# Optimization experiments

Hardware: AMD Instinct MI355X
Metric: run time of the kernel (lower is better)

The kernel has to match this reference:

```python
import jax, jax.numpy as jnp
import numpy as np
from jax import lax

B, C_IN, H, W = 32, 2048, 14, 14
C_MID = 1024
EPS = 1e-5


def _bn(x, gamma, beta, mean, var):
    # eval-mode batchnorm over channel axis 1 of NCHW
    inv = gamma / jnp.sqrt(var + EPS)
    return x * inv[None, :, None, None] + (beta - mean * inv)[None, :, None, None]


def setup_inputs() -> dict:
    key = jax.random.key(0)
    ks = jax.random.split(key, 16)
    x = jax.random.normal(ks[0], (B, C_IN, H, W), jnp.float32)
    # conv1: 3x3, 2048 -> 1024, xavier-normal init
    std1 = np.sqrt(2.0 / (C_IN * 9 + C_MID * 9)).astype(np.float32)
    w1 = jax.random.normal(ks[1], (C_MID, C_IN, 3, 3), jnp.float32) * std1
    b1 = jnp.zeros((C_MID,), jnp.float32)
    bn1_gamma = 1.0 + 0.1 * jax.random.normal(ks[2], (C_MID,), jnp.float32)
    bn1_beta = 0.1 * jax.random.normal(ks[3], (C_MID,), jnp.float32)
    bn1_mean = 0.1 * jax.random.normal(ks[4], (C_MID,), jnp.float32)
    bn1_var = jax.random.uniform(ks[5], (C_MID,), jnp.float32, 0.5, 1.5)
    # selectLayer: 1x1, 1024 -> 18 (stored as [out, in])
    std_s = np.sqrt(2.0 / (C_MID + 18)).astype(np.float32)
    w_sel = jax.random.normal(ks[6], (18, C_MID), jnp.float32) * std_s
    b_sel = jnp.zeros((18,), jnp.float32)
    # boxLayer: 1x1, 1024 -> 36, uniform(-5, 5) init
    w_box = jax.random.uniform(ks[7], (36, C_MID), jnp.float32, -5.0, 5.0)
    b_box = jnp.zeros((36,), jnp.float32)
    bnb_gamma = 1.0 + 0.1 * jax.random.normal(ks[8], (36,), jnp.float32)
    bnb_beta = 0.1 * jax.random.normal(ks[9], (36,), jnp.float32)
    bnb_mean = 0.1 * jax.random.normal(ks[10], (36,), jnp.float32)
    bnb_var = jax.random.uniform(ks[11], (36,), jnp.float32, 0.5, 1.5)
    return {
        'x': x, 'w1': w1, 'b1': b1,
        'bn1_gamma': bn1_gamma, 'bn1_beta': bn1_beta, 'bn1_mean': bn1_mean, 'bn1_var': bn1_var,
        'w_sel': w_sel, 'b_sel': b_sel,
        'w_box': w_box, 'b_box': b_box,
        'bnb_gamma': bnb_gamma, 'bnb_beta': bnb_beta, 'bnb_mean': bnb_mean, 'bnb_var': bnb_var,
    }


def reference(x, w1, b1, bn1_gamma, bn1_beta, bn1_mean, bn1_var,
              w_sel, b_sel, w_box, b_box,
              bnb_gamma, bnb_beta, bnb_mean, bnb_var):
    n = x.shape[0]
    # conv1 + BN + ReLU (3x3, padding=1)
    h = lax.conv_general_dilated(x, w1, (1, 1), 'SAME',
                                 dimension_numbers=('NCHW', 'OIHW', 'NCHW'))
    h = h + b1[None, :, None, None]
    h = jax.nn.relu(_bn(h, bn1_gamma, bn1_beta, bn1_mean, bn1_var))
    # selectLayer: 1x1 conv + ReLU -> [n, 18, H, W]
    score = jnp.einsum('nchw,oc->nohw', h, w_sel) + b_sel[None, :, None, None]
    score = jax.nn.relu(score)
    # boxLayer: 1x1 conv + BN + ReLU -> [n, 36, H, W]
    box = jnp.einsum('nchw,oc->nohw', h, w_box) + b_box[None, :, None, None]
    box = jax.nn.relu(_bn(box, bnb_gamma, bnb_beta, bnb_mean, bnb_var))
    # permute NCHW -> NHWC, reshape to anchors
    box = jnp.transpose(box, (0, 2, 3, 1)).reshape(n, -1, 4) * 419.0  # [n, 1764, 4]
    score = jnp.transpose(score, (0, 2, 3, 1)).reshape(n, -1, 2)      # [n, 1764, 2]
    score = jax.nn.softmax(score, axis=-1)
    return score, box
```

## Files before the change

kernel.cpp:

```cpp
#include <hip/hip_runtime.h>
#include <hip/hip_bf16.h>
#include <math.h>

#define CIN   2048
#define CMID  1024
#define NB    32
#define HWSP  196
#define NPOS  6272
#define WELEM 2097152
#define NSTEP 192

typedef __attribute__((ext_vector_type(4))) float f32x4;
typedef __attribute__((ext_vector_type(8))) short short8;
typedef __attribute__((ext_vector_type(4))) float float4v;

typedef const __attribute__((address_space(1))) unsigned int* as1_u32p;
typedef __attribute__((address_space(3))) unsigned int* as3_u32p;

__device__ __forceinline__ void gload_lds16(const void* g, void* l) {
  __builtin_amdgcn_global_load_lds((as1_u32p)g, (as3_u32p)l, 16, 0, 0);
}

__global__ __launch_bounds__(256) void pack_all(
    const float* __restrict__ w1, const float* __restrict__ b1,
    const float* __restrict__ g1, const float* __restrict__ be1,
    const float* __restrict__ mu1, const float* __restrict__ va1,
    const float* __restrict__ wsel, const float* __restrict__ wbox,
    const float* __restrict__ x,
    __hip_bfloat16* __restrict__ Wp, float* __restrict__ inv1,
    float* __restrict__ add1, float* __restrict__ Wh,
    __hip_bfloat16* __restrict__ Xp)
{
  __shared__ char shm[25088];
  if (blockIdx.x < 8192) {
    float* lw = (float*)shm;
    const int gid0 = blockIdx.x * 256;
    const float4v* src4 = (const float4v*)(w1 + (long)gid0 * 9);
    float4v* l4 = (float4v*)lw;
    #pragma unroll
    for (int i = 0; i < 3; ++i) {
      int idx = i * 256 + threadIdx.x;
      if (idx < 576) l4[idx] = src4[idx];
    }
    __syncthreads();
    const int gid = gid0 + threadIdx.x;
    float v[9];
    #pragma unroll
    for (int k = 0; k < 9; ++k) v[k] = lw[threadIdx.x * 9 + k];
    #pragma unroll
    for (int k = 0; k < 9; ++k)
      Wp[(long)k * WELEM + gid] = __float2bfloat16(v[k]);

    if (gid < CMID) {
      float iv = g1[gid] / sqrtf(va1[gid] + 1e-5f);
      inv1[gid] = iv;
      add1[gid] = b1[gid] * iv + be1[gid] - mu1[gid] * iv;
    }
    if (gid < CMID * 54) {
      int co = gid / 54, o = gid % 54;
      Wh[gid] = (o < 18) ? wsel[o * CMID + co] : wbox[(o - 18) * CMID + co];
    }
  } else {
    __hip_bfloat16* lx = (__hip_bfloat16*)shm;
    const int b = blockIdx.x - 8192;
    const int n = b >> 5;
    const int cc = b & 31;
    const int ci0 = cc * 64;
    const float* src = x + ((long)n * CIN + ci0) * HWSP;
    for (int i = threadIdx.x; i < 64 * HWSP; i += 256)
      lx[i] = __float2bfloat16(src[i]);
    __syncthreads();
    const int ci = threadIdx.x & 63;
    const int pq = threadIdx.x >> 6;
    __hip_bfloat16* dst = Xp + (long)n * 256 * CIN + ci0 + ci;
    const __hip_bfloat16 z = __float2bfloat16(0.f);
    #pragma unroll
    for (int k = 0; k < 64; ++k) {
      int pos = k * 4 + pq;
      int y = pos >> 4, xx = pos & 15;
      __hip_bfloat16 v = z;
      if (y >= 1 && y <= 14 && xx >= 1 && xx <= 14)
        v = lx[ci * HWSP + (y - 1) * 14 + (xx - 1)];
      dst[(long)pos * CIN] = v;
    }
  }
}

__global__ __launch_bounds__(256, 2) void conv_mfma(
    const __hip_bfloat16* __restrict__ Wp,
    const __hip_bfloat16* __restrict__ Xp,
    __hip_bfloat16* __restrict__ hout0,
    __hip_bfloat16* __restrict__ hout1,
    __hip_bfloat16* __restrict__ hout2)
{
  __shared__ char smem[2 * 24576];

  const int t = threadIdx.x;
  const int bx = blockIdx.x;
  const int r  = bx & 7;
  const int q  = bx >> 3;
  const int kidx = q >> 2;
  const int mtile = q & 3;
  int ntile;
  if (kidx < 6) {
    ntile = r + 8 * kidx;
  } else {
    if (r != ((q & 3) << 1)) return;
    ntile = 48;
  }
  const int z = blockIdx.y;
  const int lane = t & 63;
  const int wv = t >> 6;
  const int wr2 = wv >> 1;
  const int wc2 = wv & 1;

  const int srow = t >> 2;
  const int swb = ((t & 3) << 4) ^ ((srow & 6) << 3);

  const long arowbase = (long)(mtile * 256 + srow) * CIN + (swb >> 1);

  long bbase[2];
  #pragma unroll
  for (int i = 0; i < 2; ++i) {
    int jj = ntile * 128 + srow + 64 * i;
    int n0 = jj / HWSP, p0 = jj % HWSP;
    int hh = p0 / 14, ww = p0 % 14;
    bbase[i] = (long)(n0 * 256 + hh * 16 + ww) * CIN + (swb >> 1);
  }

  const int fr = lane & 15;
  const int ksl = lane >> 4;
  const int kgsw = ((ksl << 4) ^ ((fr & 6) << 3));

  f32x4 acc[8][4] = {};
  short8 a_[8], b_[4];

  const int tap0 = z * 3;

  #define STAGE(gv, bi) do {                                                    \
    int g_ = (gv);                                                              \
    int kt_ = tap0 + (g_ >> 6);                                                 \
    int ck_ = (g_ & 63) << 5;                                                   \
    int kh_ = (kt_ * 11) >> 5;                                                  \
    int kw_ = kt_ - kh_ * 3;                                                    \
    char* d_ = smem + (bi) * 24576;                                             \
    const __hip_bfloat16* ap_ = Wp + (long)kt_ * WELEM + arowbase + ck_;        \
    _Pragma("unroll")                                                           \
    for (int i_ = 0; i_ < 4; ++i_)                                              \
      gload_lds16(ap_ + (long)i_ * 64 * CIN, d_ + i_ * 4096 + t * 16);          \
    long boff_ = (long)(kh_ * 16 + kw_) * CIN + ck_;                            \
    _Pragma("unroll")                                                           \
    for (int i_ = 0; i_ < 2; ++i_)                                              \
      gload_lds16(Xp + bbase[i_] + boff_, d_ + 16384 + i_ * 4096 + t * 16);     \
  } while (0)

  #define READF(bi) do {                                                        \
    const char* cb_ = smem + (bi) * 24576;                                      \
    _Pragma("unroll")                                                           \
    for (int i = 0; i < 8; ++i)                                                 \
      a_[i] = *(const short8*)(cb_ + (wr2 * 128 + i * 16 + fr) * 64 + kgsw);    \
    _Pragma("unroll")                                                           \
    for (int i = 0; i < 4; ++i)                                                 \
      b_[i] = *(const short8*)(cb_ + 16384 + (wc2 * 64 + i * 16 + fr) * 64 + kgsw); \
  } while (0)

  #define MFMA32() do {                                                         \
    __builtin_amdgcn_s_setprio(1);                                              \
    _Pragma("unroll")                                                           \
    for (int m = 0; m < 8; ++m)                                                 \
      _Pragma("unroll")                                                         \
      for (int n = 0; n < 4; ++n)                                               \
        acc[m][n] = __builtin_amdgcn_mfma_f32_16x16x32_bf16(a_[m], b_[n], acc[m][n], 0, 0, 0); \
    __builtin_amdgcn_s_setprio(0);                                              \
  } while (0)

  #define WAITV0() asm volatile("s_waitcnt vmcnt(0)" ::: "memory")
  #define LGKM0()  asm volatile("s_waitcnt lgkmcnt(0)" ::: "memory")
  #define BAR() do { asm volatile("" ::: "memory");                             \
                     __builtin_amdgcn_s_barrier();                              \
                     asm volatile("" ::: "memory"); } while (0)

  STAGE(0, 0);
  for (int s = 0; s < NSTEP - 1; ++s) {
    WAITV0();
    LGKM0();
    BAR();
    STAGE(s + 1, (s + 1) & 1);
    READF(s & 1);
    MFMA32();
  }
  WAITV0(); LGKM0(); BAR();
  READF((NSTEP - 1) & 1);
  MFMA32();

  __hip_bfloat16* dsth = (z == 0) ? hout0 : (z == 1) ? hout1 : hout2;
  const int rg = ksl * 4;
  #pragma unroll
  for (int m = 0; m < 8; ++m) {
    const int co0 = mtile * 256 + wr2 * 128 + m * 16 + rg;
    #pragma unroll
    for (int r_ = 0; r_ < 4; ++r_) {
      const int co = co0 + r_;
      #pragma unroll
      for (int n = 0; n < 4; ++n) {
        const int j = ntile * 128 + wc2 * 64 + n * 16 + fr;
        dsth[(long)co * NPOS + j] = __float2bfloat16(acc[m][n][r_]);
      }
    }
  }
  #undef STAGE
  #undef READF
  #undef MFMA32
  #undef WAITV0
  #undef LGKM0
  #undef BAR
}

__global__ __launch_bounds__(512) void head_fused(
    const __hip_bfloat16* __restrict__ h0, const __hip_bfloat16* __restrict__ h1,
    const __hip_bfloat16* __restrict__ h2,
    const float* __restrict__ Wh,
    const float* __restrict__ inv1, const float* __restrict__ add1,
    const float* __restrict__ bsel, const float* __restrict__ bbox,
    const float* __restrict__ gb, const float* __restrict__ beb,
    const float* __restrict__ mub, const float* __restrict__ vab,
    float* __restrict__ out)
{
  __shared__ float red[4 * 64 * 54];
  const int t = threadIdx.x;
  const int jl = t & 63;
  const int cg = __builtin_amdgcn_readfirstlane(t >> 6);
  const int j0 = blockIdx.x * 64;
  const int j = j0 + jl;

  float acc[54];
  #pragma unroll
  for (int o = 0; o < 54; ++o) acc[o] = 0.f;

  const __hip_bfloat16* hp0 = h0 + (long)(cg * 128) * NPOS + j;
  const __hip_bfloat16* hp1 = h1 + (long)(cg * 128) * NPOS + j;
  const __hip_bfloat16* hp2 = h2 + (long)(cg * 128) * NPOS + j;
  const float* wp = Wh + cg * 128 * 54;
  const float* ivp = inv1 + cg * 128;
  const float* adp = add1 + cg * 128;
  for (int i = 0; i < 128; ++i) {
    float hv = __bfloat162float(hp0[(long)i * NPOS])
             + __bfloat162float(hp1[(long)i * NPOS])
             + __bfloat162float(hp2[(long)i * NPOS]);
    hv = fmaxf(hv * ivp[i] + adp[i], 0.f);
    const float* wr_ = wp + i * 54;
    #pragma unroll
    for (int o = 0; o < 54; ++o) acc[o] += hv * wr_[o];
  }
  if (cg < 4) {
    #pragma unroll
    for (int o = 0; o < 54; ++o) red[(cg * 64 + jl) * 54 + o] = acc[o];
  }
  __syncthreads();
  if (cg >= 4) {
    #pragma unroll
    for (int o = 0; o < 54; ++o) red[((cg - 4) * 64 + jl) * 54 + o] += acc[o];
  }
  __syncthreads();

  for (int idx = t; idx < 576; idx += 512) {
    int jj = idx / 9, pr = idx % 9;
    float s0 = bsel[2 * pr], s1 = bsel[2 * pr + 1];
    #pragma unroll
    for (int c = 0; c < 4; ++c) {
      s0 += red[(c * 64 + jj) * 54 + 2 * pr];
      s1 += red[(c * 64 + jj) * 54 + 2 * pr + 1];
    }
    s0 = fmaxf(s0, 0.f); s1 = fmaxf(s1, 0.f);
    float mx = fmaxf(s0, s1);
    float e0 = expf(s0 - mx), e1 = expf(s1 - mx);
    float inv = 1.f / (e0 + e1);
    int jg = j0 + jj;
    int nn = jg / HWSP, p = jg % HWSP;
    long off = ((long)nn * 1764 + p * 9 + pr) * 2;
    out[off] = e0 * inv;
    out[off + 1] = e1 * inv;
  }

  float* outb = out + (long)NB * 1764 * 2;
  for (int idx = t; idx < 2304; idx += 512) {
    int jj = idx / 36, o = idx % 36;
    float v = bbox[o];
    #pragma unroll
    for (int c = 0; c < 4; ++c) v += red[(c * 64 + jj) * 54 + 18 + o];
    float iv = gb[o] / sqrtf(vab[o] + 1e-5f);
    v = v * iv + (beb[o] - mub[o] * iv);
    v = fmaxf(v, 0.f) * 419.f;
    int jg = j0 + jj;
    int nn = jg / HWSP, p = jg % HWSP;
    outb[((long)nn * 1764 + p * 9 + (o >> 2)) * 4 + (o & 3)] = v;
  }
}

extern "C" void kernel_launch(void* const* d_in, const int* in_sizes, int n_in,
                              void* d_out, int out_size, void* d_ws, size_t ws_size,
                              hipStream_t stream) {
  const float* x    = (const float*)d_in[0];
  const float* w1   = (const float*)d_in[1];
  const float* b1   = (const float*)d_in[2];
  const float* g1   = (const float*)d_in[3];
  const float* be1  = (const float*)d_in[4];
  const float* mu1  = (const float*)d_in[5];
  const float* va1  = (const float*)d_in[6];
  const float* wsel = (const float*)d_in[7];
  const float* bsel = (const float*)d_in[8];
  const float* wbox = (const float*)d_in[9];
  const float* bbox = (const float*)d_in[10];
  const float* gb   = (const float*)d_in[11];
  const float* beb  = (const float*)d_in[12];
  const float* mub  = (const float*)d_in[13];
  const float* vab  = (const float*)d_in[14];

  char* ws = (char*)d_ws;
  __hip_bfloat16* Wp = (__hip_bfloat16*)(ws);
  __hip_bfloat16* Xp = (__hip_bfloat16*)(ws + 37748736);
  __hip_bfloat16* hb0 = (__hip_bfloat16*)(ws + 71303168);
  __hip_bfloat16* hb1 = (__hip_bfloat16*)(ws + 84148224);
  __hip_bfloat16* hb2 = (__hip_bfloat16*)(ws + 96993280);
  float* inv1        = (float*)(ws + 109838336);
  float* add1        = (float*)(ws + 109842432);
  float* Wh          = (float*)(ws + 109846528);

  hipLaunchKernelGGL(pack_all, dim3(9216), dim3(256), 0, stream,
                     w1, b1, g1, be1, mu1, va1, wsel, wbox, x, Wp, inv1, add1, Wh, Xp);
  hipLaunchKernelGGL(conv_mfma, dim3(224, 3), dim3(256), 0, stream,
                     Wp, Xp, hb0, hb1, hb2);
  hipLaunchKernelGGL(head_fused, dim3(98), dim3(512), 0, stream,
                     hb0, hb1, hb2, Wh, inv1, add1, bsel, bbox, gb, beb, mub, vab, (float*)d_out);
}
```

Measured before the change: 392.2 us.

## Triple-buffer conv LDS stages and interleave loads with split MFMA halves

The conv kernel's shared memory goes from double to triple buffering, so stage s+2 is prefetched while stage s is computed. The per-step wait relaxes from vmcnt(0) to vmcnt(6), which only requires the older stage's global-to-LDS loads to have landed. The weight and activation loads are split into separate issues, and the MFMA block is split in two halves so the activation load issues between them. This should hide more global-load latency behind matrix math, at the cost of 72KB of LDS per block, which could limit occupancy.

After: 394.2 us. About the same (+0.5%).

```diff
diff --git a/kernel.cpp b/kernel.cpp
--- a/kernel.cpp
+++ b/kernel.cpp
@@ -93,7 +93,7 @@
     __hip_bfloat16* __restrict__ hout1,
     __hip_bfloat16* __restrict__ hout2)
 {
-  __shared__ char smem[2 * 24576];
+  __shared__ char smem[3 * 24576];
 
   const int t = threadIdx.x;
   const int bx = blockIdx.x;
@@ -137,21 +137,28 @@
 
   const int tap0 = z * 3;
 
-  #define STAGE(gv, bi) do {                                                    \
+  #define STAGE_A(gv, bi) do {                                                  \
+    int g_ = (gv);                                                              \
+    int kt_ = tap0 + (g_ >> 6);                                                 \
+    int ck_ = (g_ & 63) << 5;                                                   \
+    char* d_ = smem + (bi) * 24576;                                             \
+    const __hip_bfloat16* ap_ = Wp + (long)kt_ * WELEM + arowbase + ck_;        \
+    _Pragma("unroll")                                                           \
+    for (int i_ = 0; i_ < 4; ++i_)                                              \
+      gload_lds16(ap_ + (long)i_ * 64 * CIN, d_ + i_ * 4096 + t * 16);          \
+  } while (0)
+
+  #define STAGE_B(gv, bi) do {                                                  \
     int g_ = (gv);                                                              \
     int kt_ = tap0 + (g_ >> 6);                                                 \
     int ck_ = (g_ & 63) << 5;                                                   \
     int kh_ = (kt_ * 11) >> 5;                                                  \
     int kw_ = kt_ - kh_ * 3;                                                    \
-    char* d_ = smem + (bi) * 24576;                                             \
-    const __hip_bfloat16* ap_ = Wp + (long)kt_ * WELEM + arowbase + ck_;        \
-    _Pragma("unroll")                                                           \
-    for (int i_ = 0; i_ < 4; ++i_)                                              \
-      gload_lds16(ap_ + (long)i_ * 64 * CIN, d_ + i_ * 4096 + t * 16);          \
+    char* d_ = smem + (bi) * 24576 + 16384;                                     \
     long boff_ = (long)(kh_ * 16 + kw_) * CIN + ck_;                            \
     _Pragma("unroll")                                                           \
     for (int i_ = 0; i_ < 2; ++i_)                                              \
-      gload_lds16(Xp + bbase[i_] + boff_, d_ + 16384 + i_ * 4096 + t * 16);     \
+      gload_lds16(Xp + bbase[i_] + boff_, d_ + i_ * 4096 + t * 16);             \
   } while (0)
 
   #define READF(bi) do {                                                        \
@@ -164,34 +171,54 @@
       b_[i] = *(const short8*)(cb_ + 16384 + (wc2 * 64 + i * 16 + fr) * 64 + kgsw); \
   } while (0)
 
-  #define MFMA32() do {                                                         \
+  #define MFMA_LO() do {                                                        \
     __builtin_amdgcn_s_setprio(1);                                              \
     _Pragma("unroll")                                                           \
-    for (int m = 0; m < 8; ++m)                                                 \
+    for (int m = 0; m < 4; ++m)                                                 \
       _Pragma("unroll")                                                         \
       for (int n = 0; n < 4; ++n)                                               \
         acc[m][n] = __builtin_amdgcn_mfma_f32_16x16x32_bf16(a_[m], b_[n], acc[m][n], 0, 0, 0); \
     __builtin_amdgcn_s_setprio(0);                                              \
   } while (0)
 
+  #define MFMA_HI() do {                                                        \
+    __builtin_amdgcn_s_setprio(1);                                              \
+    _Pragma("unroll")                                                           \
+    for (int m = 4; m < 8; ++m)                                                 \
+      _Pragma("unroll")                                                         \
+      for (int n = 0; n < 4; ++n)                                               \
+        acc[m][n] = __builtin_amdgcn_mfma_f32_16x16x32_bf16(a_[m], b_[n], acc[m][n], 0, 0, 0); \
+    __builtin_amdgcn_s_setprio(0);                                              \
+  } while (0)
+
+  #define WAITV6() asm volatile("s_waitcnt vmcnt(6)" ::: "memory")
   #define WAITV0() asm volatile("s_waitcnt vmcnt(0)" ::: "memory")
-  #define LGKM0()  asm volatile("s_waitcnt lgkmcnt(0)" ::: "memory")
   #define BAR() do { asm volatile("" ::: "memory");                             \
                      __builtin_amdgcn_s_barrier();                              \
                      asm volatile("" ::: "memory"); } while (0)
 
-  STAGE(0, 0);
-  for (int s = 0; s < NSTEP - 1; ++s) {
-    WAITV0();
-    LGKM0();
+  STAGE_A(0, 0); STAGE_B(0, 0);
+  STAGE_A(1, 1); STAGE_B(1, 1);
+
+  int bc = 0, bs = 2;
+  for (int s = 0; s < NSTEP - 2; ++s) {
+    WAITV6();
     BAR();
-    STAGE(s + 1, (s + 1) & 1);
-    READF(s & 1);
-    MFMA32();
-  }
-  WAITV0(); LGKM0(); BAR();
-  READF((NSTEP - 1) & 1);
-  MFMA32();
+    STAGE_A(s + 2, bs);
+    READF(bc);
+    MFMA_LO();
+    STAGE_B(s + 2, bs);
+    MFMA_HI();
+    bc = (bc == 2) ? 0 : bc + 1;
+    bs = (bs == 2) ? 0 : bs + 1;
+  }
+  WAITV6(); BAR();
+  READF(bc);
+  MFMA_LO(); MFMA_HI();
+  bc = (bc == 2) ? 0 : bc + 1;
+  WAITV0(); BAR();
+  READF(bc);
+  MFMA_LO(); MFMA_HI();
 
   __hip_bfloat16* dsth = (z == 0) ? hout0 : (z == 1) ? hout1 : hout2;
   const int rg = ksl * 4;
@@ -208,11 +235,13 @@
       }
     }
   }
-  #undef STAGE
+  #undef STAGE_A
+  #undef STAGE_B
   #undef READF
-  #undef MFMA32
+  #undef MFMA_LO
+  #undef MFMA_HI
+  #undef WAITV6
   #undef WAITV0
-  #undef LGKM0
   #undef BAR
 }
 
```
